# Kernel tuning notes

Measured on AMD Instinct MI355X. Metric: run time of the kernel, lower is better.

Reference implementation:

```python
import jax, jax.numpy as jnp
import numpy as np

H = 1024
F = 3584
E = 8
TOP_K = 2
B, S = 2, 1024


def setup_inputs() -> dict:
    key = jax.random.key(0)
    ks = jax.random.split(key, 5)
    scale_h = 1.0 / np.sqrt(H)
    scale_f = 1.0 / np.sqrt(F)
    return {
        "hidden_states": jax.random.normal(ks[0], (B, S, H), dtype=jnp.float32),
        "gate_w": jax.random.normal(ks[1], (H, E), dtype=jnp.float32) * scale_h,
        "w1": jax.random.normal(ks[2], (E, H, F), dtype=jnp.float32) * scale_h,
        "w3": jax.random.normal(ks[3], (E, H, F), dtype=jnp.float32) * scale_h,
        "w2": jax.random.normal(ks[4], (E, F, H), dtype=jnp.float32) * scale_f,
        "top_k": TOP_K,
    }


def reference(hidden_states, gate_w, w1, w3, w2, top_k):
    b, s, h = hidden_states.shape
    e = gate_w.shape[1]
    x = hidden_states.reshape(-1, h)  # [N, H]

    # Router: softmax over experts, top-k selection, renormalize (Mixtral).
    logits = x @ gate_w                             # [N, E]
    probs = jax.nn.softmax(logits, axis=-1)
    rw, sel = jax.lax.top_k(probs, top_k)           # [N, K]
    rw = rw / jnp.sum(rw, axis=-1, keepdims=True)

    # Dispatch/combine weights: combine[n, e] = sum_k rw[n,k] * (sel[n,k]==e).
    # This is the mathematical equivalent of moe_permute + weighted moe_unpermute.
    combine = jnp.sum(jax.nn.one_hot(sel, e, dtype=rw.dtype) * rw[..., None], axis=1)  # [N, E]

    # Grouped SwiGLU expert MLPs; loop over the small fixed expert count so the
    # [N, F] intermediate is materialized one expert at a time.
    out = jnp.zeros_like(x)
    for ei in range(e):
        hdn = jax.nn.silu(x @ w1[ei]) * (x @ w3[ei])  # [N, F]
        out = out + combine[:, ei:ei + 1] * (hdn @ w2[ei])
    return out.reshape(b, s, h)
```

## Files before the change

### kernel.cpp

```cpp
#include <hip/hip_runtime.h>
#include <hip/hip_bf16.h>

#define NTOK 2048
#define HD   1024
#define FD   3584
#define NE   8

#define BM 128
#define BN1 64
#define BM2 64
#define BN 128
#define BK 64
#define NIT1 (HD / BK)
#define KS2 2
#define KLEN2 (FD / KS2)
#define NIT2 (KLEN2 / BK)

typedef __attribute__((ext_vector_type(8))) short short8;
typedef __attribute__((ext_vector_type(4))) float f32x4;

__device__ __forceinline__ unsigned short f2bf(float f) {
    __hip_bfloat16 h = __float2bfloat16(f);
    union { __hip_bfloat16 h; unsigned short u; } c; c.h = h;
    return c.u;
}

typedef __attribute__((address_space(1))) const unsigned int g_cu32;
typedef __attribute__((address_space(3))) unsigned int l_u32;
__device__ __forceinline__ void gl16(const void* g, void* l) {
    __builtin_amdgcn_global_load_lds((g_cu32*)g, (l_u32*)(unsigned int)(size_t)l, 16, 0, 0);
}

__global__ void k_router(const float* __restrict__ x, const float* __restrict__ gw,
                         int* __restrict__ sel, float* __restrict__ selw,
                         int* __restrict__ counts) {
    int token = blockIdx.x * 4 + (threadIdx.x >> 6);
    int lane  = threadIdx.x & 63;
    if (token >= NTOK) return;
    const float* xr = x + (size_t)token * HD;
    float acc[NE];
#pragma unroll
    for (int e = 0; e < NE; e++) acc[e] = 0.f;
    for (int h = lane; h < HD; h += 64) {
        float xv = xr[h];
        const float4* g = (const float4*)(gw + (size_t)h * NE);
        float4 g0 = g[0], g1 = g[1];
        acc[0] += xv * g0.x; acc[1] += xv * g0.y; acc[2] += xv * g0.z; acc[3] += xv * g0.w;
        acc[4] += xv * g1.x; acc[5] += xv * g1.y; acc[6] += xv * g1.z; acc[7] += xv * g1.w;
    }
#pragma unroll
    for (int e = 0; e < NE; e++) {
#pragma unroll
        for (int off = 32; off >= 1; off >>= 1) acc[e] += __shfl_xor(acc[e], off, 64);
    }
    if (lane == 0) {
        float m = acc[0];
#pragma unroll
        for (int e = 1; e < NE; e++) m = fmaxf(m, acc[e]);
        float z[NE];
#pragma unroll
        for (int e = 0; e < NE; e++) z[e] = expf(acc[e] - m);
        int e0 = 0; float z0 = z[0];
#pragma unroll
        for (int e = 1; e < NE; e++) if (z[e] > z0) { z0 = z[e]; e0 = e; }
        int e1 = -1; float z1 = -1.f;
#pragma unroll
        for (int e = 0; e < NE; e++) if (e != e0 && z[e] > z1) { z1 = z[e]; e1 = e; }
        float s = z0 + z1;
        sel[token * 2 + 0] = e0; sel[token * 2 + 1] = e1;
        selw[token * 2 + 0] = z0 / s; selw[token * 2 + 1] = z1 / s;
        atomicAdd(&counts[e0], 1);
        atomicAdd(&counts[e1], 1);
    }
}

__global__ void k_scan(const int* __restrict__ counts, int* __restrict__ basep,
                       int* __restrict__ fillc) {
    if (threadIdx.x == 0 && blockIdx.x == 0) {
        int b = 0;
        for (int e = 0; e < NE; e++) { basep[e] = b; b += counts[e]; fillc[e] = 0; }
    }
}

__global__ void k_fill(const int* __restrict__ sel, const float* __restrict__ selw,
                       const int* __restrict__ basep, int* __restrict__ fillc,
                       int* __restrict__ rowmap, int* __restrict__ rowk,
                       float* __restrict__ roww) {
    int n = blockIdx.x * blockDim.x + threadIdx.x;
    if (n >= NTOK) return;
#pragma unroll
    for (int k = 0; k < 2; k++) {
        int e = sel[n * 2 + k];
        int p = atomicAdd(&fillc[e], 1);
        int g = basep[e] + p;
        rowmap[g] = n; rowk[g] = k; roww[g] = selw[n * 2 + k];
    }
}

__global__ void k_cvt(const float* __restrict__ x, unsigned short* __restrict__ xb) {
    size_t i = ((size_t)blockIdx.x * blockDim.x + threadIdx.x) * 8;
    float4 a = *(const float4*)(x + i);
    float4 b = *(const float4*)(x + i + 4);
    unsigned short p[8] __attribute__((aligned(16))) =
        { f2bf(a.x), f2bf(a.y), f2bf(a.z), f2bf(a.w),
          f2bf(b.x), f2bf(b.y), f2bf(b.z), f2bf(b.w) };
    *(uint4*)(xb + i) = *(uint4*)p;
}

__global__ void k_wt3(const float* __restrict__ w1, const float* __restrict__ w3,
                      const float* __restrict__ w2,
                      unsigned short* __restrict__ w1t, unsigned short* __restrict__ w3t,
                      unsigned short* __restrict__ w2t) {
    __shared__ unsigned short tile[64][66];
    const int z = blockIdx.z;
    int K, N, tx, ty;
    const float* src;
    unsigned short* dst;
    if (z < 16) {
        K = HD; N = FD;
        const int e = z & 7;
        src = (z < 8 ? w1 : w3) + (size_t)e * K * N;
        dst = (z < 8 ? w1t : w3t) + (size_t)e * N * K;
        tx = blockIdx.x % (FD / 64); ty = blockIdx.x / (FD / 64);
    } else {
        K = FD; N = HD;
        const int e = z - 16;
        src = w2 + (size_t)e * K * N;
        dst = w2t + (size_t)e * N * K;
        tx = blockIdx.x % (HD / 64); ty = blockIdx.x / (HD / 64);
    }
    src += (size_t)(ty * 64) * N + tx * 64;
    dst += (size_t)(tx * 64) * K + ty * 64;

    const int t = threadIdx.x;
    {
        const int r = t >> 4;
        const int c4 = (t & 15) * 4;
#pragma unroll
        for (int i = 0; i < 4; i++) {
            const int kr = r + i * 16;
            float4 v = *(const float4*)(src + (size_t)kr * N + c4);
            unsigned short p[4] = { f2bf(v.x), f2bf(v.y), f2bf(v.z), f2bf(v.w) };
            *(unsigned int*)&tile[kr][c4]     = *(unsigned int*)&p[0];
            *(unsigned int*)&tile[kr][c4 + 2] = *(unsigned int*)&p[2];
        }
    }
    __syncthreads();
    const int n = t >> 3;
    const int kc = (t & 7) * 8;
#pragma unroll
    for (int i = 0; i < 2; i++) {
        const int nn = n + i * 32;
        unsigned short p[8] __attribute__((aligned(16)));
#pragma unroll
        for (int j = 0; j < 8; j++) p[j] = tile[kc + j][nn];
        *(uint4*)&dst[(size_t)nn * K + kc] = *(uint4*)p;
    }
}

__global__ __launch_bounds__(256, 2) void k_gemm1(
    const unsigned short* __restrict__ xb,
    const unsigned short* __restrict__ w1t, const unsigned short* __restrict__ w3t,
    const int* __restrict__ counts, const int* __restrict__ basep,
    const int* __restrict__ rowmap, unsigned short* __restrict__ act)
{
    const int e = blockIdx.z;
    const int nrows = counts[e];
    const int m0 = blockIdx.y * BM;
    if (m0 >= nrows) return;
    const int f0 = blockIdx.x * BN1;
    const int gbase = basep[e];

    __shared__ __align__(16) unsigned short At[2][BM][BK];
    __shared__ __align__(16) unsigned short B1[2][BN1][BK];
    __shared__ __align__(16) unsigned short B3[2][BN1][BK];

    const int t = threadIdx.x;
    const int lane = t & 63;
    const int w = t >> 6;
    const int wrm = w >> 1, wnn = w & 1;
    const int lr = lane >> 3;
    const int so = ((lane & 7) ^ lr) * 8;

    const unsigned short* asrc[4];
#pragma unroll
    for (int c = 0; c < 4; c++) {
        const int row = (w * 4 + c) * 8 + lr;
        const int tok = rowmap[gbase + min(m0 + row, nrows - 1)];
        asrc[c] = xb + (size_t)tok * HD + so;
    }
    const unsigned short* b1src[2];
    const unsigned short* b3src[2];
#pragma unroll
    for (int c = 0; c < 2; c++) {
        const int row = (w * 2 + c) * 8 + lr;
        b1src[c] = w1t + ((size_t)(e * FD + f0 + row)) * HD + so;
        b3src[c] = w3t + ((size_t)(e * FD + f0 + row)) * HD + so;
    }

    f32x4 acc1[4][2], acc3[4][2];
#pragma unroll
    for (int i = 0; i < 4; i++)
#pragma unroll
        for (int j = 0; j < 2; j++) { acc1[i][j] = (f32x4)(0.f); acc3[i][j] = (f32x4)(0.f); }

    const int l15 = lane & 15;
    const int lhi = lane >> 4;
    const int rs = (l15 & 7) * 8;

#pragma unroll
    for (int c = 0; c < 4; c++) gl16(asrc[c], &At[0][(w * 4 + c) * 8][0]);
#pragma unroll
    for (int c = 0; c < 2; c++) {
        gl16(b1src[c], &B1[0][(w * 2 + c) * 8][0]);
        gl16(b3src[c], &B3[0][(w * 2 + c) * 8][0]);
    }

    for (int it = 0; it < NIT1; ++it) {
        const int cur = it & 1;
        if (it + 1 < NIT1) {
            const int kn = (it + 1) * BK;
#pragma unroll
            for (int c = 0; c < 4; c++) gl16(asrc[c] + kn, &At[cur ^ 1][(w * 4 + c) * 8][0]);
#pragma unroll
            for (int c = 0; c < 2; c++) {
                gl16(b1src[c] + kn, &B1[cur ^ 1][(w * 2 + c) * 8][0]);
                gl16(b3src[c] + kn, &B3[cur ^ 1][(w * 2 + c) * 8][0]);
            }
            asm volatile("s_waitcnt vmcnt(8)" ::: "memory");
        } else {
            asm volatile("s_waitcnt vmcnt(0)" ::: "memory");
        }
        __builtin_amdgcn_s_barrier();
#pragma unroll
        for (int kk = 0; kk < 2; kk++) {
            const int kc = (kk * 32 + lhi * 8) ^ rs;
            short8 af[4], b1f[2], b3f[2];
#pragma unroll
            for (int i = 0; i < 4; i++)
                af[i] = *(const short8*)&At[cur][wrm * 64 + i * 16 + l15][kc];
#pragma unroll
            for (int j = 0; j < 2; j++) {
                b1f[j] = *(const short8*)&B1[cur][wnn * 32 + j * 16 + l15][kc];
                b3f[j] = *(const short8*)&B3[cur][wnn * 32 + j * 16 + l15][kc];
            }
#pragma unroll
            for (int i = 0; i < 4; i++)
#pragma unroll
                for (int j = 0; j < 2; j++) {
                    acc1[i][j] = __builtin_amdgcn_mfma_f32_16x16x32_bf16(af[i], b1f[j], acc1[i][j], 0, 0, 0);
                    acc3[i][j] = __builtin_amdgcn_mfma_f32_16x16x32_bf16(af[i], b3f[j], acc3[i][j], 0, 0, 0);
                }
        }
        __builtin_amdgcn_s_barrier();
    }

    const int rbase = wrm * 64 + lhi * 4;
    const int cbase = f0 + wnn * 32 + l15;
#pragma unroll
    for (int i = 0; i < 4; i++) {
#pragma unroll
        for (int r = 0; r < 4; r++) {
            const int ml = rbase + i * 16 + r;
            if (m0 + ml < nrows) {
                const size_t rowoff = (size_t)(gbase + m0 + ml) * FD;
#pragma unroll
                for (int j = 0; j < 2; j++) {
                    float y1 = acc1[i][j][r];
                    float y3 = acc3[i][j][r];
                    float sv = (y1 / (1.f + __expf(-y1))) * y3;
                    act[rowoff + cbase + j * 16] = f2bf(sv);
                }
            }
        }
    }
}

__global__ __launch_bounds__(256, 4) void k_gemm2(
    const unsigned short* __restrict__ act,
    const unsigned short* __restrict__ w2t,
    const int* __restrict__ counts, const int* __restrict__ basep,
    const int* __restrict__ rowmap, const int* __restrict__ rowk,
    const float* __restrict__ roww, float* __restrict__ partial)
{
    const int z = blockIdx.z;
    const int e = z >> 1, ks = z & 1;
    const int nrows = counts[e];
    const int m0 = blockIdx.y * BM2;
    if (m0 >= nrows) return;
    const int h0 = blockIdx.x * BN;
    const int gbase = basep[e];
    const int kbase = ks * KLEN2;

    __shared__ __align__(16) unsigned short At[2][BM2][BK];
    __shared__ __align__(16) unsigned short Bt[2][BN][BK];

    const int t = threadIdx.x;
    const int lane = t & 63;
    const int w = t >> 6;
    const int wr2 = w >> 1, wn2 = w & 1;
    const int lr = lane >> 3;
    const int so = ((lane & 7) ^ lr) * 8;

    const unsigned short* asrc[2];
#pragma unroll
    for (int c = 0; c < 2; c++) {
        const int row = (w * 2 + c) * 8 + lr;
        asrc[c] = act + ((size_t)gbase + min(m0 + row, nrows - 1)) * FD + so + kbase;
    }
    const unsigned short* bsrc[4];
#pragma unroll
    for (int c = 0; c < 4; c++) {
        const int row = (w * 4 + c) * 8 + lr;
        bsrc[c] = w2t + ((size_t)(e * HD + h0 + row)) * FD + so + kbase;
    }

    f32x4 acc[2][4];
#pragma unroll
    for (int i = 0; i < 2; i++)
#pragma unroll
        for (int j = 0; j < 4; j++) acc[i][j] = (f32x4)(0.f);

    const int l15 = lane & 15;
    const int lhi = lane >> 4;
    const int rs = (l15 & 7) * 8;

#pragma unroll
    for (int c = 0; c < 2; c++) gl16(asrc[c], &At[0][(w * 2 + c) * 8][0]);
#pragma unroll
    for (int c = 0; c < 4; c++) gl16(bsrc[c], &Bt[0][(w * 4 + c) * 8][0]);

    for (int it = 0; it < NIT2; ++it) {
        const int cur = it & 1;
        if (it + 1 < NIT2) {
            const int kn = (it + 1) * BK;
#pragma unroll
            for (int c = 0; c < 2; c++) gl16(asrc[c] + kn, &At[cur ^ 1][(w * 2 + c) * 8][0]);
#pragma unroll
            for (int c = 0; c < 4; c++) gl16(bsrc[c] + kn, &Bt[cur ^ 1][(w * 4 + c) * 8][0]);
            asm volatile("s_waitcnt vmcnt(6)" ::: "memory");
        } else {
            asm volatile("s_waitcnt vmcnt(0)" ::: "memory");
        }
        __builtin_amdgcn_s_barrier();
#pragma unroll
        for (int kk = 0; kk < 2; kk++) {
            const int kc = (kk * 32 + lhi * 8) ^ rs;
            short8 af[2], bf[4];
#pragma unroll
            for (int i = 0; i < 2; i++)
                af[i] = *(const short8*)&At[cur][wr2 * 32 + i * 16 + l15][kc];
#pragma unroll
            for (int j = 0; j < 4; j++)
                bf[j] = *(const short8*)&Bt[cur][wn2 * 64 + j * 16 + l15][kc];
#pragma unroll
            for (int i = 0; i < 2; i++)
#pragma unroll
                for (int j = 0; j < 4; j++)
                    acc[i][j] = __builtin_amdgcn_mfma_f32_16x16x32_bf16(af[i], bf[j], acc[i][j], 0, 0, 0);
        }
        __builtin_amdgcn_s_barrier();
    }

    const int rbase = wr2 * 32 + lhi * 4;
    const int cbase = h0 + wn2 * 64 + l15;
#pragma unroll
    for (int i = 0; i < 2; i++) {
#pragma unroll
        for (int r = 0; r < 4; r++) {
            const int ml = rbase + i * 16 + r;
            if (m0 + ml < nrows) {
                const int grow = gbase + m0 + ml;
                const int tok = rowmap[grow];
                const int slot = rowk[grow];
                const float wv = roww[grow];
                float* op = partial + (((size_t)slot * KS2 + ks) * NTOK + tok) * HD + cbase;
#pragma unroll
                for (int j = 0; j < 4; j++) op[j * 16] = acc[i][j][r] * wv;
            }
        }
    }
}

__global__ void k_combine(const float* __restrict__ partial, float* __restrict__ out) {
    size_t i = ((size_t)blockIdx.x * blockDim.x + threadIdx.x) * 4;
    const size_t st = (size_t)NTOK * HD;
    float4 o = *(const float4*)(partial + i);
#pragma unroll
    for (int s = 1; s < 2 * KS2; s++) {
        float4 v = *(const float4*)(partial + (size_t)s * st + i);
        o.x += v.x; o.y += v.y; o.z += v.z; o.w += v.w;
    }
    *(float4*)(out + i) = o;
}

extern "C" void kernel_launch(void* const* d_in, const int* in_sizes, int n_in,
                              void* d_out, int out_size, void* d_ws, size_t ws_size,
                              hipStream_t stream) {
    const float* x  = (const float*)d_in[0];
    const float* gw = (const float*)d_in[1];
    const float* w1 = (const float*)d_in[2];
    const float* w3 = (const float*)d_in[3];
    const float* w2 = (const float*)d_in[4];
    float* out = (float*)d_out;

    char* ws = (char*)d_ws;
    size_t off = 0;
    auto alloc = [&](size_t b) { char* p = ws + off; off += (b + 255) & ~(size_t)255; return p; };
    int*   sel    = (int*)  alloc((size_t)NTOK * 2 * 4);
    float* selw   = (float*)alloc((size_t)NTOK * 2 * 4);
    int*   counts = (int*)  alloc(NE * 4);
    int*   basep  = (int*)  alloc(NE * 4);
    int*   fillc  = (int*)  alloc(NE * 4);
    int*   rowmap = (int*)  alloc((size_t)NTOK * 2 * 4);
    int*   rowk   = (int*)  alloc((size_t)NTOK * 2 * 4);
    float* roww   = (float*)alloc((size_t)NTOK * 2 * 4);
    unsigned short* xb  = (unsigned short*)alloc((size_t)NTOK * HD * 2);
    unsigned short* act = (unsigned short*)alloc((size_t)NTOK * 2 * FD * 2);
    unsigned short* w1t = (unsigned short*)alloc((size_t)NE * HD * FD * 2);
    unsigned short* w3t = (unsigned short*)alloc((size_t)NE * HD * FD * 2);
    unsigned short* w2t = (unsigned short*)alloc((size_t)NE * HD * FD * 2);
    float* partial = (float*)w1t;

    hipMemsetAsync(counts, 0, NE * 4, stream);
    k_wt3<<<dim3(896, 1, 24), 256, 0, stream>>>(w1, w3, w2, w1t, w3t, w2t);
    k_cvt<<<(NTOK * HD) / (256 * 8), 256, 0, stream>>>(x, xb);
    k_router<<<NTOK / 4, 256, 0, stream>>>(x, gw, sel, selw, counts);
    k_scan<<<1, 64, 0, stream>>>(counts, basep, fillc);
    k_fill<<<NTOK / 256, 256, 0, stream>>>(sel, selw, basep, fillc, rowmap, rowk, roww);
    k_gemm1<<<dim3(FD / BN1, NTOK / BM, NE), 256, 0, stream>>>(xb, w1t, w3t, counts, basep, rowmap, act);
    k_gemm2<<<dim3(HD / BN, NTOK / BM2, NE * KS2), 256, 0, stream>>>(act, w2t, counts, basep, rowmap, rowk, roww, partial);
    k_combine<<<(NTOK * HD) / (256 * 4), 256, 0, stream>>>(partial, out);
}
```

Before: 330.6 us.

## Fuse weight bf16 conversion and transpose into expert GEMM tile loads

```diff
diff --git a/kernel.cpp b/kernel.cpp
--- a/kernel.cpp
+++ b/kernel.cpp
@@ -107,60 +107,9 @@
     *(uint4*)(xb + i) = *(uint4*)p;
 }
 
-__global__ void k_wt3(const float* __restrict__ w1, const float* __restrict__ w3,
-                      const float* __restrict__ w2,
-                      unsigned short* __restrict__ w1t, unsigned short* __restrict__ w3t,
-                      unsigned short* __restrict__ w2t) {
-    __shared__ unsigned short tile[64][66];
-    const int z = blockIdx.z;
-    int K, N, tx, ty;
-    const float* src;
-    unsigned short* dst;
-    if (z < 16) {
-        K = HD; N = FD;
-        const int e = z & 7;
-        src = (z < 8 ? w1 : w3) + (size_t)e * K * N;
-        dst = (z < 8 ? w1t : w3t) + (size_t)e * N * K;
-        tx = blockIdx.x % (FD / 64); ty = blockIdx.x / (FD / 64);
-    } else {
-        K = FD; N = HD;
-        const int e = z - 16;
-        src = w2 + (size_t)e * K * N;
-        dst = w2t + (size_t)e * N * K;
-        tx = blockIdx.x % (HD / 64); ty = blockIdx.x / (HD / 64);
-    }
-    src += (size_t)(ty * 64) * N + tx * 64;
-    dst += (size_t)(tx * 64) * K + ty * 64;
-
-    const int t = threadIdx.x;
-    {
-        const int r = t >> 4;
-        const int c4 = (t & 15) * 4;
-#pragma unroll
-        for (int i = 0; i < 4; i++) {
-            const int kr = r + i * 16;
-            float4 v = *(const float4*)(src + (size_t)kr * N + c4);
-            unsigned short p[4] = { f2bf(v.x), f2bf(v.y), f2bf(v.z), f2bf(v.w) };
-            *(unsigned int*)&tile[kr][c4]     = *(unsigned int*)&p[0];
-            *(unsigned int*)&tile[kr][c4 + 2] = *(unsigned int*)&p[2];
-        }
-    }
-    __syncthreads();
-    const int n = t >> 3;
-    const int kc = (t & 7) * 8;
-#pragma unroll
-    for (int i = 0; i < 2; i++) {
-        const int nn = n + i * 32;
-        unsigned short p[8] __attribute__((aligned(16)));
-#pragma unroll
-        for (int j = 0; j < 8; j++) p[j] = tile[kc + j][nn];
-        *(uint4*)&dst[(size_t)nn * K + kc] = *(uint4*)p;
-    }
-}
-
 __global__ __launch_bounds__(256, 2) void k_gemm1(
     const unsigned short* __restrict__ xb,
-    const unsigned short* __restrict__ w1t, const unsigned short* __restrict__ w3t,
+    const float* __restrict__ w1, const float* __restrict__ w3,
     const int* __restrict__ counts, const int* __restrict__ basep,
     const int* __restrict__ rowmap, unsigned short* __restrict__ act)
 {
@@ -189,14 +138,14 @@
         const int tok = rowmap[gbase + min(m0 + row, nrows - 1)];
         asrc[c] = xb + (size_t)tok * HD + so;
     }
-    const unsigned short* b1src[2];
-    const unsigned short* b3src[2];
-#pragma unroll
-    for (int c = 0; c < 2; c++) {
-        const int row = (w * 2 + c) * 8 + lr;
-        b1src[c] = w1t + ((size_t)(e * FD + f0 + row)) * HD + so;
-        b3src[c] = w3t + ((size_t)(e * FD + f0 + row)) * HD + so;
-    }
+
+    const int nq = t & 15;
+    const int kd = t >> 4;
+    const float* b1p = w1 + (size_t)e * HD * FD + (size_t)(4 * kd) * FD + f0 + 4 * nq;
+    const float* b3p = w3 + (size_t)e * HD * FD + (size_t)(4 * kd) * FD + f0 + 4 * nq;
+    unsigned int* const b1w = (unsigned int*)&B1[0][0][0];
+    unsigned int* const b3w = (unsigned int*)&B3[0][0][0];
+    const int BUFW = BN1 * BK / 2;
 
     f32x4 acc1[4][2], acc3[4][2];
 #pragma unroll
@@ -208,30 +157,50 @@
     const int lhi = lane >> 4;
     const int rs = (l15 & 7) * 8;
 
+    float4 b1v[4], b3v[4];
+
+#define G1_WRITE_B(buf_) do {                                                   \
+    _Pragma("unroll")                                                           \
+    for (int c = 0; c < 4; c++) {                                               \
+        const int n = 4 * nq + c;                                               \
+        const int wi = n * 32 + 4 * ((kd >> 1) ^ (n & 7)) + 2 * (kd & 1);       \
+        uint2 u;                                                                \
+        u.x = (unsigned int)f2bf(((const float*)&b1v[0])[c])                    \
+            | ((unsigned int)f2bf(((const float*)&b1v[1])[c]) << 16);           \
+        u.y = (unsigned int)f2bf(((const float*)&b1v[2])[c])                    \
+            | ((unsigned int)f2bf(((const float*)&b1v[3])[c]) << 16);           \
+        *(uint2*)&b1w[(buf_) * BUFW + wi] = u;                                  \
+        uint2 v;                                                                \
+        v.x = (unsigned int)f2bf(((const float*)&b3v[0])[c])                    \
+            | ((unsigned int)f2bf(((const float*)&b3v[1])[c]) << 16);           \
+        v.y = (unsigned int)f2bf(((const float*)&b3v[2])[c])                    \
+            | ((unsigned int)f2bf(((const float*)&b3v[3])[c]) << 16);           \
+        *(uint2*)&b3w[(buf_) * BUFW + wi] = v;                                  \
+    }                                                                           \
+} while (0)
+
+#pragma unroll
+    for (int r = 0; r < 4; r++) b1v[r] = *(const float4*)(b1p + (size_t)r * FD);
+#pragma unroll
+    for (int r = 0; r < 4; r++) b3v[r] = *(const float4*)(b3p + (size_t)r * FD);
 #pragma unroll
     for (int c = 0; c < 4; c++) gl16(asrc[c], &At[0][(w * 4 + c) * 8][0]);
-#pragma unroll
-    for (int c = 0; c < 2; c++) {
-        gl16(b1src[c], &B1[0][(w * 2 + c) * 8][0]);
-        gl16(b3src[c], &B3[0][(w * 2 + c) * 8][0]);
-    }
+    G1_WRITE_B(0);
+    asm volatile("s_waitcnt vmcnt(0)" ::: "memory");
+    __builtin_amdgcn_s_barrier();
 
     for (int it = 0; it < NIT1; ++it) {
         const int cur = it & 1;
-        if (it + 1 < NIT1) {
-            const int kn = (it + 1) * BK;
-#pragma unroll
-            for (int c = 0; c < 4; c++) gl16(asrc[c] + kn, &At[cur ^ 1][(w * 4 + c) * 8][0]);
-#pragma unroll
-            for (int c = 0; c < 2; c++) {
-                gl16(b1src[c] + kn, &B1[cur ^ 1][(w * 2 + c) * 8][0]);
-                gl16(b3src[c] + kn, &B3[cur ^ 1][(w * 2 + c) * 8][0]);
-            }
-            asm volatile("s_waitcnt vmcnt(8)" ::: "memory");
-        } else {
-            asm volatile("s_waitcnt vmcnt(0)" ::: "memory");
-        }
-        __builtin_amdgcn_s_barrier();
+        const bool more = (it + 1 < NIT1);
+        if (more) {
+            const size_t k0 = (size_t)(it + 1) * BK;
+#pragma unroll
+            for (int r = 0; r < 4; r++) b1v[r] = *(const float4*)(b1p + (k0 + r) * FD);
+#pragma unroll
+            for (int r = 0; r < 4; r++) b3v[r] = *(const float4*)(b3p + (k0 + r) * FD);
+#pragma unroll
+            for (int c = 0; c < 4; c++) gl16(asrc[c] + k0, &At[cur ^ 1][(w * 4 + c) * 8][0]);
+        }
 #pragma unroll
         for (int kk = 0; kk < 2; kk++) {
             const int kc = (kk * 32 + lhi * 8) ^ rs;
@@ -251,6 +220,10 @@
                     acc1[i][j] = __builtin_amdgcn_mfma_f32_16x16x32_bf16(af[i], b1f[j], acc1[i][j], 0, 0, 0);
                     acc3[i][j] = __builtin_amdgcn_mfma_f32_16x16x32_bf16(af[i], b3f[j], acc3[i][j], 0, 0, 0);
                 }
+        }
+        if (more) {
+            G1_WRITE_B(cur ^ 1);
+            asm volatile("s_waitcnt vmcnt(0)" ::: "memory");
         }
         __builtin_amdgcn_s_barrier();
     }
@@ -274,11 +247,12 @@
             }
         }
     }
-}
-
-__global__ __launch_bounds__(256, 4) void k_gemm2(
+#undef G1_WRITE_B
+}
+
+__global__ __launch_bounds__(256, 3) void k_gemm2(
     const unsigned short* __restrict__ act,
-    const unsigned short* __restrict__ w2t,
+    const float* __restrict__ w2,
     const int* __restrict__ counts, const int* __restrict__ basep,
     const int* __restrict__ rowmap, const int* __restrict__ rowk,
     const float* __restrict__ roww, float* __restrict__ partial)
@@ -308,12 +282,12 @@
         const int row = (w * 2 + c) * 8 + lr;
         asrc[c] = act + ((size_t)gbase + min(m0 + row, nrows - 1)) * FD + so + kbase;
     }
-    const unsigned short* bsrc[4];
-#pragma unroll
-    for (int c = 0; c < 4; c++) {
-        const int row = (w * 4 + c) * 8 + lr;
-        bsrc[c] = w2t + ((size_t)(e * HD + h0 + row)) * FD + so + kbase;
-    }
+
+    const int nq = t & 31;
+    const int kd8 = t >> 5;
+    const float* bp = w2 + (size_t)e * FD * HD + (size_t)(kbase + 4 * kd8) * HD + h0 + 4 * nq;
+    unsigned int* const btw = (unsigned int*)&Bt[0][0][0];
+    const int BUFW2 = BN * BK / 2;
 
     f32x4 acc[2][4];
 #pragma unroll
@@ -325,24 +299,50 @@
     const int lhi = lane >> 4;
     const int rs = (l15 & 7) * 8;
 
+    float4 bv[2][4];
+
+#define G2_WRITE_B(buf_) do {                                                   \
+    _Pragma("unroll")                                                           \
+    for (int s = 0; s < 2; s++) {                                               \
+        const int kdv = kd8 + 8 * s;                                            \
+        _Pragma("unroll")                                                       \
+        for (int c = 0; c < 4; c++) {                                           \
+            const int n = 4 * nq + c;                                           \
+            const int wi = n * 32 + 4 * ((kdv >> 1) ^ (n & 7)) + 2 * (kdv & 1); \
+            uint2 u;                                                            \
+            u.x = (unsigned int)f2bf(((const float*)&bv[s][0])[c])              \
+                | ((unsigned int)f2bf(((const float*)&bv[s][1])[c]) << 16);     \
+            u.y = (unsigned int)f2bf(((const float*)&bv[s][2])[c])              \
+                | ((unsigned int)f2bf(((const float*)&bv[s][3])[c]) << 16);     \
+            *(uint2*)&btw[(buf_) * BUFW2 + wi] = u;                             \
+        }                                                                       \
+    }                                                                           \
+} while (0)
+
+#pragma unroll
+    for (int s = 0; s < 2; s++)
+#pragma unroll
+        for (int r = 0; r < 4; r++)
+            bv[s][r] = *(const float4*)(bp + (size_t)(32 * s + r) * HD);
 #pragma unroll
     for (int c = 0; c < 2; c++) gl16(asrc[c], &At[0][(w * 2 + c) * 8][0]);
-#pragma unroll
-    for (int c = 0; c < 4; c++) gl16(bsrc[c], &Bt[0][(w * 4 + c) * 8][0]);
+    G2_WRITE_B(0);
+    asm volatile("s_waitcnt vmcnt(0)" ::: "memory");
+    __builtin_amdgcn_s_barrier();
 
     for (int it = 0; it < NIT2; ++it) {
         const int cur = it & 1;
-        if (it + 1 < NIT2) {
-            const int kn = (it + 1) * BK;
-#pragma unroll
-            for (int c = 0; c < 2; c++) gl16(asrc[c] + kn, &At[cur ^ 1][(w * 2 + c) * 8][0]);
-#pragma unroll
-            for (int c = 0; c < 4; c++) gl16(bsrc[c] + kn, &Bt[cur ^ 1][(w * 4 + c) * 8][0]);
-            asm volatile("s_waitcnt vmcnt(6)" ::: "memory");
-        } else {
-            asm volatile("s_waitcnt vmcnt(0)" ::: "memory");
-        }
-        __builtin_amdgcn_s_barrier();
+        const bool more = (it + 1 < NIT2);
+        if (more) {
+            const size_t k0 = (size_t)(it + 1) * BK;
+#pragma unroll
+            for (int s = 0; s < 2; s++)
+#pragma unroll
+                for (int r = 0; r < 4; r++)
+                    bv[s][r] = *(const float4*)(bp + (k0 + 32 * s + r) * HD);
+#pragma unroll
+            for (int c = 0; c < 2; c++) gl16(asrc[c] + k0, &At[cur ^ 1][(w * 2 + c) * 8][0]);
+        }
 #pragma unroll
         for (int kk = 0; kk < 2; kk++) {
             const int kc = (kk * 32 + lhi * 8) ^ rs;
@@ -358,6 +358,10 @@
 #pragma unroll
                 for (int j = 0; j < 4; j++)
                     acc[i][j] = __builtin_amdgcn_mfma_f32_16x16x32_bf16(af[i], bf[j], acc[i][j], 0, 0, 0);
+        }
+        if (more) {
+            G2_WRITE_B(cur ^ 1);
+            asm volatile("s_waitcnt vmcnt(0)" ::: "memory");
         }
         __builtin_amdgcn_s_barrier();
     }
@@ -380,6 +384,7 @@
             }
         }
     }
+#undef G2_WRITE_B
 }
 
 __global__ void k_combine(const float* __restrict__ partial, float* __restrict__ out) {
@@ -417,18 +422,14 @@
     float* roww   = (float*)alloc((size_t)NTOK * 2 * 4);
     unsigned short* xb  = (unsigned short*)alloc((size_t)NTOK * HD * 2);
     unsigned short* act = (unsigned short*)alloc((size_t)NTOK * 2 * FD * 2);
-    unsigned short* w1t = (unsigned short*)alloc((size_t)NE * HD * FD * 2);
-    unsigned short* w3t = (unsigned short*)alloc((size_t)NE * HD * FD * 2);
-    unsigned short* w2t = (unsigned short*)alloc((size_t)NE * HD * FD * 2);
-    float* partial = (float*)w1t;
+    float* partial = (float*)alloc((size_t)2 * KS2 * NTOK * HD * 4);
 
     hipMemsetAsync(counts, 0, NE * 4, stream);
-    k_wt3<<<dim3(896, 1, 24), 256, 0, stream>>>(w1, w3, w2, w1t, w3t, w2t);
     k_cvt<<<(NTOK * HD) / (256 * 8), 256, 0, stream>>>(x, xb);
     k_router<<<NTOK / 4, 256, 0, stream>>>(x, gw, sel, selw, counts);
     k_scan<<<1, 64, 0, stream>>>(counts, basep, fillc);
     k_fill<<<NTOK / 256, 256, 0, stream>>>(sel, selw, basep, fillc, rowmap, rowk, roww);
-    k_gemm1<<<dim3(FD / BN1, NTOK / BM, NE), 256, 0, stream>>>(xb, w1t, w3t, counts, basep, rowmap, act);
-    k_gemm2<<<dim3(HD / BN, NTOK / BM2, NE * KS2), 256, 0, stream>>>(act, w2t, counts, basep, rowmap, rowk, roww, partial);
+    k_gemm1<<<dim3(FD / BN1, NTOK / BM, NE), 256, 0, stream>>>(xb, w1, w3, counts, basep, rowmap, act);
+    k_gemm2<<<dim3(HD / BN, NTOK / BM2, NE * KS2), 256, 0, stream>>>(act, w2, counts, basep, rowmap, rowk, roww, partial);
     k_combine<<<(NTOK * HD) / (256 * 4), 256, 0, stream>>>(partial, out);
 }
```

Result: slower. 393.2 us (+18.9%).
